# Kernel optimization log

Hardware: AMD Instinct MI355X
Metric: run time of the kernel (lower is better)

The kernel has to match this reference:

```python
import jax, jax.numpy as jnp
import numpy as np

N_NODES = 100000


def setup_inputs() -> dict:
    key = jax.random.key(0)
    k1, k2, k3, k4 = jax.random.split(key, 4)
    E = 1600000
    D_IN, D_OUT = 128, 128
    feat = jax.random.normal(k1, (N_NODES, D_IN), dtype=jnp.float32)
    src = jax.random.randint(k2, (E,), 0, N_NODES, dtype=jnp.int32)
    dst = jax.random.randint(k3, (E,), 0, N_NODES, dtype=jnp.int32)
    # xavier_uniform for weight [in, out]
    limit = float(np.sqrt(6.0 / (D_IN + D_OUT)))
    weight = jax.random.uniform(k4, (D_IN, D_OUT), dtype=jnp.float32,
                                minval=-limit, maxval=limit)
    bias = jnp.zeros((D_OUT,), dtype=jnp.float32)
    return {"feat": feat, "weight": weight, "bias": bias, "src": src, "dst": dst}


def reference(feat, weight, bias, src, dst):
    # in-degree normalization: norm_i = 1/sqrt(in_deg(i)); clamp deg>=1 to avoid inf
    deg = jax.ops.segment_sum(jnp.ones(src.shape[0], dtype=jnp.float32), dst,
                              num_segments=N_NODES)
    norm = jax.lax.rsqrt(jnp.maximum(deg, 1.0))[:, None]  # [N,1]
    h = feat * norm
    # update_all(copy_src, sum): scatter-sum src features into dst nodes (SpMM)
    agg = jax.ops.segment_sum(h[src], dst, num_segments=N_NODES)  # [N, D_in]
    # in_feats == out_feats -> aggregate first, then dense transform
    rst = agg @ weight          # [N, D_out]
    rst = rst * norm + bias
    return rst
```

## Files before the change

kernel.cpp:

```cpp
#include <hip/hip_runtime.h>


constexpr int N_NODES = 100000;
constexpr int D = 128;
constexpr int NB = 256;
constexpr int GROUP = (N_NODES + NB - 1) / NB;
constexpr int CAP = 14336;
constexpr int CONVB = 1280;

typedef float f32x4 __attribute__((ext_vector_type(4)));
typedef short short8 __attribute__((ext_vector_type(8)));
typedef unsigned uint4v __attribute__((ext_vector_type(4)));

__device__ __forceinline__ ushort f2bf(float x) {
    unsigned u = __float_as_uint(x);
    return (ushort)((u + 0x7fffu + ((u >> 16) & 1u)) >> 16);
}
__device__ __forceinline__ float bf2f(ushort h) {
    return __uint_as_float(((unsigned)h) << 16);
}

__global__ __launch_bounds__(256) void p1_histo_conv(const int* __restrict__ dst, int E,
                                                     int* __restrict__ bhist,
                                                     const float* __restrict__ W,
                                                     ushort* __restrict__ whi,
                                                     ushort* __restrict__ wlo,
                                                     const float* __restrict__ feat,
                                                     uint2* __restrict__ ft2) {
    int t = threadIdx.x, blk = blockIdx.x;
    if (blk >= NB) {
        int base = (blk - NB) * 256 + t;
        int stride = CONVB * 256;
        for (int i = base; i < N_NODES * 32; i += stride) {
            f32x4 v = ((const f32x4*)feat)[i];
            uint2 o;
            o.x = (unsigned)f2bf(v[0]) | ((unsigned)f2bf(v[1]) << 16);
            o.y = (unsigned)f2bf(v[2]) | ((unsigned)f2bf(v[3]) << 16);
            ft2[i] = o;
        }
        return;
    }
    __shared__ int h[NB];
    h[t] = 0;
    if (blk < 64) {
        int p = blk * 256 + t;
        int i  = p & 7;
        int l  = (p >> 3) & 63;
        int kt = (p >> 9) & 3;
        int ct = (p >> 11);
        int k = kt * 32 + (l >> 4) * 8 + i;
        int n = ct * 16 + (l & 15);
        float x = W[k * 128 + n];
        ushort hh = f2bf(x);
        whi[p] = hh;
        wlo[p] = f2bf(x - bf2f(hh));
    }
    __syncthreads();
    int per = (E + NB - 1) / NB;
    int s = blk * per, e = min(E, s + per);
    for (int i = s + t; i < e; i += 256) atomicAdd(&h[dst[i] / GROUP], 1);
    __syncthreads();
    bhist[t * NB + blk] = h[t];
}

__global__ __launch_bounds__(256) void p1_scanrow(int* __restrict__ bhist,
                                                  int* __restrict__ rowtot) {
    __shared__ int lds[256];
    int b = blockIdx.x, t = threadIdx.x;
    int v = bhist[b * NB + t];
    lds[t] = v; __syncthreads();
    for (int off = 1; off < 256; off <<= 1) {
        int x = (t >= off) ? lds[t - off] : 0;
        __syncthreads();
        lds[t] += x;
        __syncthreads();
    }
    bhist[b * NB + t] = lds[t] - v;
    if (t == 255) rowtot[b] = lds[255];
}

__global__ __launch_bounds__(256) void p1_scatter(const int* __restrict__ src,
                                                  const int* __restrict__ dst, int E,
                                                  const int* __restrict__ bhist,
                                                  const int* __restrict__ rowtot,
                                                  int* __restrict__ pairs) {
    __shared__ int loff[NB];
    __shared__ int bb[NB];
    int t = threadIdx.x, blk = blockIdx.x;
    int rv = rowtot[t];
    bb[t] = rv; __syncthreads();
    for (int off = 1; off < 256; off <<= 1) {
        int x = (t >= off) ? bb[t - off] : 0;
        __syncthreads();
        bb[t] += x;
        __syncthreads();
    }
    loff[t] = bhist[t * NB + blk] + bb[t] - rv;
    __syncthreads();
    int per = (E + NB - 1) / NB;
    int s = blk * per, e = min(E, s + per);
    for (int i = s + t; i < e; i += 256) {
        int d = dst[i];
        int b = d / GROUP;
        int pos = atomicAdd(&loff[b], 1);
        pairs[pos] = ((d - b * GROUP) << 17) | src[i];
    }
}

__global__ __launch_bounds__(256) void p2_all(const int* __restrict__ pairs,
                                              const int* __restrict__ rowtot,
                                              int* __restrict__ deg,
                                              int* __restrict__ offs,
                                              float* __restrict__ norm,
                                              int* __restrict__ esrc) {
    __shared__ int h[512];
    __shared__ int ssum[256];
    __shared__ int bb[256];
    __shared__ int sbuf[CAP];
    int t = threadIdx.x, b = blockIdx.x;
    int lo = b * GROUP;
    int cnt = min(GROUP, N_NODES - lo);

    int rv = rowtot[t];
    bb[t] = rv;
    h[t] = 0; h[t + 256] = 0;
    __syncthreads();
    for (int off = 1; off < 256; off <<= 1) {
        int x = (t >= off) ? bb[t - off] : 0;
        __syncthreads();
        bb[t] += x;
        __syncthreads();
    }
    int s1 = bb[b];
    int s0 = s1 - rowtot[b];
    __syncthreads();

    for (int i = s0 + t; i < s1; i += 256) atomicAdd(&h[pairs[i] >> 17], 1);
    __syncthreads();

    int v0 = h[2 * t], v1 = h[2 * t + 1];
    int s = v0 + v1;
    ssum[t] = s; __syncthreads();
    for (int off = 1; off < 256; off <<= 1) {
        int x = (t >= off) ? ssum[t - off] : 0;
        __syncthreads();
        ssum[t] += x;
        __syncthreads();
    }
    int pre = ssum[t] - s;
    if (2 * t < cnt) {
        int node = lo + 2 * t;
        deg[node] = v0;
        offs[node] = s0 + pre;
        norm[node] = rsqrtf(fmaxf((float)v0, 1.0f));
    }
    if (2 * t + 1 < cnt) {
        int node = lo + 2 * t + 1;
        deg[node] = v1;
        offs[node] = s0 + pre + v0;
        norm[node] = rsqrtf(fmaxf((float)v1, 1.0f));
    }
    __syncthreads();
    h[2 * t] = pre;
    h[2 * t + 1] = pre + v0;
    __syncthreads();

    int wsize = s1 - s0;
    bool fits = (wsize <= CAP);
    for (int i = s0 + t; i < s1; i += 256) {
        int p = pairs[i];
        int dl = p >> 17;
        int sv = p & 0x1FFFF;
        int pos = atomicAdd(&h[dl], 1);
        if (fits) sbuf[pos] = sv; else esrc[s0 + pos] = sv;
    }
    __syncthreads();
    if (fits)
        for (int i = t; i < wsize; i += 256) esrc[s0 + i] = sbuf[i];
}

__global__ __launch_bounds__(256) void k_gather16(const unsigned* __restrict__ ft,
                                                  const int* __restrict__ offs,
                                                  const int* __restrict__ deg,
                                                  const int* __restrict__ esrc,
                                                  const float* __restrict__ norm,
                                                  unsigned* __restrict__ outbf) {
    int gtid = blockIdx.x * blockDim.x + threadIdx.x;
    int node = gtid >> 6;
    if (node >= N_NODES) return;
    int lane = gtid & 63;
    int g  = lane >> 4;
    int sl = lane & 15;
    int start = offs[node];
    int cnt   = deg[node];
    int last  = start + cnt - 1;
    float acc[8] = {0.f, 0.f, 0.f, 0.f, 0.f, 0.f, 0.f, 0.f};
    const uint4v* ftv = (const uint4v*)ft;
    for (int j = 0; j < cnt; j += 16) {
        int i0 = start + j + g;
        int s0v = esrc[min(i0,      last)];
        int s1v = esrc[min(i0 + 4,  last)];
        int s2v = esrc[min(i0 + 8,  last)];
        int s3v = esrc[min(i0 + 12, last)];
        float w0 = (j + g      < cnt) ? norm[s0v] : 0.0f;
        float w1 = (j + g + 4  < cnt) ? norm[s1v] : 0.0f;
        float w2 = (j + g + 8  < cnt) ? norm[s2v] : 0.0f;
        float w3 = (j + g + 12 < cnt) ? norm[s3v] : 0.0f;
        uint4v u0 = ftv[(size_t)s0v * 16 + sl];
        uint4v u1 = ftv[(size_t)s1v * 16 + sl];
        uint4v u2 = ftv[(size_t)s2v * 16 + sl];
        uint4v u3 = ftv[(size_t)s3v * 16 + sl];
        #pragma unroll
        for (int q = 0; q < 4; ++q) {
            unsigned a = u0[q];
            acc[q * 2]     = fmaf(__uint_as_float(a << 16),         w0, acc[q * 2]);
            acc[q * 2 + 1] = fmaf(__uint_as_float(a & 0xffff0000u), w0, acc[q * 2 + 1]);
        }
        #pragma unroll
        for (int q = 0; q < 4; ++q) {
            unsigned a = u1[q];
            acc[q * 2]     = fmaf(__uint_as_float(a << 16),         w1, acc[q * 2]);
            acc[q * 2 + 1] = fmaf(__uint_as_float(a & 0xffff0000u), w1, acc[q * 2 + 1]);
        }
        #pragma unroll
        for (int q = 0; q < 4; ++q) {
            unsigned a = u2[q];
            acc[q * 2]     = fmaf(__uint_as_float(a << 16),         w2, acc[q * 2]);
            acc[q * 2 + 1] = fmaf(__uint_as_float(a & 0xffff0000u), w2, acc[q * 2 + 1]);
        }
        #pragma unroll
        for (int q = 0; q < 4; ++q) {
            unsigned a = u3[q];
            acc[q * 2]     = fmaf(__uint_as_float(a << 16),         w3, acc[q * 2]);
            acc[q * 2 + 1] = fmaf(__uint_as_float(a & 0xffff0000u), w3, acc[q * 2 + 1]);
        }
    }
    #pragma unroll
    for (int q = 0; q < 8; ++q) {
        acc[q] += __shfl_xor(acc[q], 16, 64);
        acc[q] += __shfl_xor(acc[q], 32, 64);
    }
    if (g == 0) {
        uint4v o;
        #pragma unroll
        for (int q = 0; q < 4; ++q)
            o[q] = (unsigned)f2bf(acc[q * 2]) | ((unsigned)f2bf(acc[q * 2 + 1]) << 16);
        ((uint4v*)outbf)[(size_t)node * 16 + sl] = o;
    }
}

__global__ __launch_bounds__(256) void k_gemm_bf(const ushort* __restrict__ aggbf,
                                                 const ushort* __restrict__ whi,
                                                 const ushort* __restrict__ wlo,
                                                 const float* __restrict__ bias,
                                                 const float* __restrict__ norm,
                                                 float* __restrict__ out) {
    __shared__ ushort sH[16384];
    __shared__ ushort sL[16384];
    {
        const short8* gh = (const short8*)whi;
        const short8* gl = (const short8*)wlo;
        short8* lh = (short8*)sH;
        short8* ll = (short8*)sL;
        for (int i = threadIdx.x; i < 2048; i += 256) { lh[i] = gh[i]; ll[i] = gl[i]; }
    }
    __syncthreads();

    const int lane = threadIdx.x & 63;
    const int wid  = threadIdx.x >> 6;
    const int rsub = lane & 15;
    const int kgrp = lane >> 4;

    const short8* BH = (const short8*)sH;
    const short8* BL = (const short8*)sL;

    const int nstrips = N_NODES / 16;
    for (int strip = blockIdx.x * 4 + wid; strip < nstrips; strip += gridDim.x * 4) {
        const int row0 = strip * 16;
        const ushort* arow = aggbf + (size_t)(row0 + rsub) * D + kgrp * 8;
        short8 a[4];
        #pragma unroll
        for (int kt = 0; kt < 4; ++kt) a[kt] = *(const short8*)(arow + kt * 32);
        float nr[4];
        #pragma unroll
        for (int r = 0; r < 4; ++r) nr[r] = norm[row0 + kgrp * 4 + r];

        #pragma unroll
        for (int ct = 0; ct < 8; ++ct) {
            f32x4 acc = {0.f, 0.f, 0.f, 0.f};
            #pragma unroll
            for (int kt = 0; kt < 4; ++kt) {
                acc = __builtin_amdgcn_mfma_f32_16x16x32_bf16(a[kt], BH[(ct * 4 + kt) * 64 + lane], acc, 0, 0, 0);
                acc = __builtin_amdgcn_mfma_f32_16x16x32_bf16(a[kt], BL[(ct * 4 + kt) * 64 + lane], acc, 0, 0, 0);
            }
            const float bc = bias[ct * 16 + rsub];
            float* ocol = out + (size_t)row0 * D + ct * 16 + rsub;
            #pragma unroll
            for (int r = 0; r < 4; ++r) {
                int row = kgrp * 4 + r;
                ocol[(size_t)row * D] = acc[r] * nr[r] + bc;
            }
        }
    }
}

__global__ void k_scatter(const float* __restrict__ feat, const int* __restrict__ src,
                          const int* __restrict__ dst, const float* __restrict__ norm,
                          int E, float* __restrict__ agg) {
    long long gtid = (long long)blockIdx.x * blockDim.x + threadIdx.x;
    int e    = (int)(gtid >> 6);
    int lane = (int)(gtid & 63);
    if (e >= E) return;
    int s = src[e];
    int t = dst[e];
    float ns = norm[s];
    float2 v = ((const float2*)(feat + (size_t)s * D))[lane];
    float* arow = agg + (size_t)t * D + lane * 2;
    atomicAdd(arow + 0, v.x * ns);
    atomicAdd(arow + 1, v.y * ns);
}
__global__ void k_deg_f(const int* __restrict__ dst, int E, float* __restrict__ deg) {
    int i = blockIdx.x * blockDim.x + threadIdx.x;
    if (i < E) atomicAdd(deg + dst[i], 1.0f);
}
__global__ void k_norm_f(float* __restrict__ dn) {
    int i = blockIdx.x * blockDim.x + threadIdx.x;
    if (i < N_NODES) dn[i] = rsqrtf(fmaxf(dn[i], 1.0f));
}
__global__ __launch_bounds__(256) void k_gemm(float* __restrict__ io,
                                              const float* __restrict__ W,
                                              const float* __restrict__ bias,
                                              const float* __restrict__ norm) {
    __shared__ float sW[D * D];
    __shared__ float srow[2][D];
    for (int i = threadIdx.x; i < D * D; i += 256) sW[i] = W[i];
    const int r = threadIdx.x >> 7;
    const int c = threadIdx.x & 127;
    const float bc = bias[c];
    const int npairs = N_NODES / 2;
    for (int rp = blockIdx.x; rp < npairs; rp += gridDim.x) {
        __syncthreads();
        const int row = rp * 2 + r;
        srow[r][c] = io[(size_t)row * D + c];
        __syncthreads();
        float acc = 0.f;
        #pragma unroll 8
        for (int k = 0; k < D; ++k)
            acc = fmaf(srow[r][k], sW[k * D + c], acc);
        io[(size_t)row * D + c] = acc * norm[row] + bc;
    }
}

extern "C" void kernel_launch(void* const* d_in, const int* in_sizes, int n_in,
                              void* d_out, int out_size, void* d_ws, size_t ws_size,
                              hipStream_t stream) {
    const float* feat   = (const float*)d_in[0];
    const float* weight = (const float*)d_in[1];
    const float* bias   = (const float*)d_in[2];
    const int*   src    = (const int*)d_in[3];
    const int*   dst    = (const int*)d_in[4];
    const int E = in_sizes[3];

    int* pairs = (int*)d_out;

    uintptr_t cur = (uintptr_t)d_ws;
    auto take = [&](size_t bytes) -> void* {
        uintptr_t r = (cur + 63) & ~(uintptr_t)63;
        cur = r + bytes;
        return (void*)r;
    };

    size_t S_ft  = (size_t)N_NODES * 64 * 4;
    size_t S_agg = (size_t)N_NODES * D * 2;
    size_t need  = S_ft + S_agg +
                   (size_t)(3 * N_NODES + 256 + NB * NB + E) * 4 + 65536 + 1024;

    unsigned* ft     = (unsigned*)take(S_ft);
    ushort*   aggbf  = (ushort*)take(S_agg);
    float*    norm   = (float*)take((size_t)N_NODES * 4);
    int*      deg    = (int*)take((size_t)N_NODES * 4);
    int*      offs   = (int*)take((size_t)N_NODES * 4);
    int*      rowtot = (int*)take(256 * 4);
    int*      bhist  = (int*)take((size_t)NB * NB * 4);
    int*      esrc   = (int*)take((size_t)E * 4);
    ushort*   whi    = (ushort*)take(16384 * 2);
    ushort*   wlo    = (ushort*)take(16384 * 2);

    if (ws_size >= need) {
        p1_histo_conv<<<NB + CONVB, 256, 0, stream>>>(dst, E, bhist, weight, whi, wlo,
                                                      feat, (uint2*)ft);
        p1_scanrow<<<NB, 256, 0, stream>>>(bhist, rowtot);
        p1_scatter<<<NB, 256, 0, stream>>>(src, dst, E, bhist, rowtot, pairs);
        p2_all<<<NB, 256, 0, stream>>>(pairs, rowtot, deg, offs, norm, esrc);
        long long gthreads = (long long)N_NODES * 64;
        k_gather16<<<(int)((gthreads + 255) / 256), 256, 0, stream>>>(ft, offs, deg, esrc,
                                                                      norm, (unsigned*)aggbf);
        k_gemm_bf<<<1024, 256, 0, stream>>>(aggbf, whi, wlo, bias, norm, (float*)d_out);
    } else {
        float* agg = (float*)d_out;
        hipMemsetAsync(d_out, 0, (size_t)N_NODES * D * sizeof(float), stream);
        hipMemsetAsync(norm, 0, (size_t)N_NODES * sizeof(float), stream);
        k_deg_f<<<(E + 255) / 256, 256, 0, stream>>>(dst, E, (float*)norm);
        k_norm_f<<<(N_NODES + 255) / 256, 256, 0, stream>>>((float*)norm);
        long long sthreads = (long long)E * 64;
        k_scatter<<<(int)((sthreads + 255) / 256), 256, 0, stream>>>(feat, src, dst, (float*)norm, E, agg);
        k_gemm<<<4096, 256, 0, stream>>>(agg, weight, bias, (float*)norm);
    }
}
```

Measured before the change: 139.0 us.

## Pack fp16 source norm into edge indices and fold row scan into histogram

The scanrow kernel is removed. Row totals are now accumulated with atomics in the histogram kernel, and each scatter block computes its column prefix by serially summing the bhist entries of all earlier blocks. A new pass packs each edge's source norm as fp16 into the upper 15 bits of its esrc entry, so the gather no longer does a dependent random load of norm[src]. In exchange it adds a memset, an extra pass over all edges, an O(NB) loop per scatter thread, and reduced precision on the norm weights, since the top bit of the half is dropped and only positive values are assumed.

```diff
diff --git a/kernel.cpp b/kernel.cpp
--- a/kernel.cpp
+++ b/kernel.cpp
@@ -1,4 +1,5 @@
 #include <hip/hip_runtime.h>
+#include <hip/hip_fp16.h>
 
 
 constexpr int N_NODES = 100000;
@@ -19,9 +20,15 @@
 __device__ __forceinline__ float bf2f(ushort h) {
     return __uint_as_float(((unsigned)h) << 16);
 }
+__device__ __forceinline__ float dec_h15(int p) {
+    unsigned short b = (unsigned short)((unsigned)p >> 17);
+    __half hh; __builtin_memcpy(&hh, &b, 2);
+    return __half2float(hh);
+}
 
 __global__ __launch_bounds__(256) void p1_histo_conv(const int* __restrict__ dst, int E,
                                                      int* __restrict__ bhist,
+                                                     int* __restrict__ rowtot,
                                                      const float* __restrict__ W,
                                                      ushort* __restrict__ whi,
                                                      ushort* __restrict__ wlo,
@@ -60,23 +67,8 @@
     int s = blk * per, e = min(E, s + per);
     for (int i = s + t; i < e; i += 256) atomicAdd(&h[dst[i] / GROUP], 1);
     __syncthreads();
-    bhist[t * NB + blk] = h[t];
-}
-
-__global__ __launch_bounds__(256) void p1_scanrow(int* __restrict__ bhist,
-                                                  int* __restrict__ rowtot) {
-    __shared__ int lds[256];
-    int b = blockIdx.x, t = threadIdx.x;
-    int v = bhist[b * NB + t];
-    lds[t] = v; __syncthreads();
-    for (int off = 1; off < 256; off <<= 1) {
-        int x = (t >= off) ? lds[t - off] : 0;
-        __syncthreads();
-        lds[t] += x;
-        __syncthreads();
-    }
-    bhist[b * NB + t] = lds[t] - v;
-    if (t == 255) rowtot[b] = lds[255];
+    bhist[blk * NB + t] = h[t];
+    if (h[t]) atomicAdd(&rowtot[t], h[t]);
 }
 
 __global__ __launch_bounds__(256) void p1_scatter(const int* __restrict__ src,
@@ -95,7 +87,9 @@
         bb[t] += x;
         __syncthreads();
     }
-    loff[t] = bhist[t * NB + blk] + bb[t] - rv;
+    int cp = 0;
+    for (int c = 0; c < blk; ++c) cp += bhist[c * NB + t];
+    loff[t] = cp + bb[t] - rv;
     __syncthreads();
     int per = (E + NB - 1) / NB;
     int s = blk * per, e = min(E, s + per);
@@ -179,11 +173,20 @@
         for (int i = t; i < wsize; i += 256) esrc[s0 + i] = sbuf[i];
 }
 
+__global__ void k_enorm(int* __restrict__ esrc, const float* __restrict__ norm, int E) {
+    int i = blockIdx.x * blockDim.x + threadIdx.x;
+    if (i < E) {
+        int s = esrc[i];
+        __half hh = __float2half(norm[s]);
+        unsigned short b; __builtin_memcpy(&b, &hh, 2);
+        esrc[i] = ((int)b << 17) | s;
+    }
+}
+
 __global__ __launch_bounds__(256) void k_gather16(const unsigned* __restrict__ ft,
                                                   const int* __restrict__ offs,
                                                   const int* __restrict__ deg,
                                                   const int* __restrict__ esrc,
-                                                  const float* __restrict__ norm,
                                                   unsigned* __restrict__ outbf) {
     int gtid = blockIdx.x * blockDim.x + threadIdx.x;
     int node = gtid >> 6;
@@ -198,14 +201,18 @@
     const uint4v* ftv = (const uint4v*)ft;
     for (int j = 0; j < cnt; j += 16) {
         int i0 = start + j + g;
-        int s0v = esrc[min(i0,      last)];
-        int s1v = esrc[min(i0 + 4,  last)];
-        int s2v = esrc[min(i0 + 8,  last)];
-        int s3v = esrc[min(i0 + 12, last)];
-        float w0 = (j + g      < cnt) ? norm[s0v] : 0.0f;
-        float w1 = (j + g + 4  < cnt) ? norm[s1v] : 0.0f;
-        float w2 = (j + g + 8  < cnt) ? norm[s2v] : 0.0f;
-        float w3 = (j + g + 12 < cnt) ? norm[s3v] : 0.0f;
+        int p0 = esrc[min(i0,      last)];
+        int p1 = esrc[min(i0 + 4,  last)];
+        int p2 = esrc[min(i0 + 8,  last)];
+        int p3 = esrc[min(i0 + 12, last)];
+        int s0v = p0 & 0x1FFFF;
+        int s1v = p1 & 0x1FFFF;
+        int s2v = p2 & 0x1FFFF;
+        int s3v = p3 & 0x1FFFF;
+        float w0 = (j + g      < cnt) ? dec_h15(p0) : 0.0f;
+        float w1 = (j + g + 4  < cnt) ? dec_h15(p1) : 0.0f;
+        float w2 = (j + g + 8  < cnt) ? dec_h15(p2) : 0.0f;
+        float w3 = (j + g + 12 < cnt) ? dec_h15(p3) : 0.0f;
         uint4v u0 = ftv[(size_t)s0v * 16 + sl];
         uint4v u1 = ftv[(size_t)s1v * 16 + sl];
         uint4v u2 = ftv[(size_t)s2v * 16 + sl];
@@ -387,14 +394,15 @@
     ushort*   wlo    = (ushort*)take(16384 * 2);
 
     if (ws_size >= need) {
-        p1_histo_conv<<<NB + CONVB, 256, 0, stream>>>(dst, E, bhist, weight, whi, wlo,
+        hipMemsetAsync(rowtot, 0, 256 * sizeof(int), stream);
+        p1_histo_conv<<<NB + CONVB, 256, 0, stream>>>(dst, E, bhist, rowtot, weight, whi, wlo,
                                                       feat, (uint2*)ft);
-        p1_scanrow<<<NB, 256, 0, stream>>>(bhist, rowtot);
         p1_scatter<<<NB, 256, 0, stream>>>(src, dst, E, bhist, rowtot, pairs);
         p2_all<<<NB, 256, 0, stream>>>(pairs, rowtot, deg, offs, norm, esrc);
+        k_enorm<<<(E + 255) / 256, 256, 0, stream>>>(esrc, norm, E);
         long long gthreads = (long long)N_NODES * 64;
         k_gather16<<<(int)((gthreads + 255) / 256), 256, 0, stream>>>(ft, offs, deg, esrc,
-                                                                      norm, (unsigned*)aggbf);
+                                                                      (unsigned*)aggbf);
         k_gemm_bf<<<1024, 256, 0, stream>>>(aggbf, whi, wlo, bias, norm, (float*)d_out);
     } else {
         float* agg = (float*)d_out;
```

Result: slower. 178.7 us (+28.5%).

## Fuse neighbor gather and bf16 MFMA GEMM into one kernel via LDS tile

Applied to the files above, without the earlier changes.

Merges the gather-aggregate kernel and the dense GEMM kernel into one. Each block aggregates 16 nodes, four per wave, into a padded LDS bf16 tile. After a barrier, each wave computes two 16-column output tiles with MFMA, reading the weight fragments directly from global memory instead of staging them in LDS. This removes the round trip of the bf16 aggregate buffer through global memory and one kernel launch. The cost is less latency hiding per wave during the gather, the block-wide barrier, and repeated global loads of the weights in every block.

```diff
diff --git a/kernel.cpp b/kernel.cpp
--- a/kernel.cpp
+++ b/kernel.cpp
@@ -7,6 +7,7 @@
 constexpr int GROUP = (N_NODES + NB - 1) / NB;
 constexpr int CAP = 14336;
 constexpr int CONVB = 1280;
+constexpr int RPAD = 136;
 
 typedef float f32x4 __attribute__((ext_vector_type(4)));
 typedef short short8 __attribute__((ext_vector_type(8)));
@@ -179,127 +180,112 @@
         for (int i = t; i < wsize; i += 256) esrc[s0 + i] = sbuf[i];
 }
 
-__global__ __launch_bounds__(256) void k_gather16(const unsigned* __restrict__ ft,
-                                                  const int* __restrict__ offs,
-                                                  const int* __restrict__ deg,
-                                                  const int* __restrict__ esrc,
-                                                  const float* __restrict__ norm,
-                                                  unsigned* __restrict__ outbf) {
-    int gtid = blockIdx.x * blockDim.x + threadIdx.x;
-    int node = gtid >> 6;
-    if (node >= N_NODES) return;
-    int lane = gtid & 63;
-    int g  = lane >> 4;
-    int sl = lane & 15;
-    int start = offs[node];
-    int cnt   = deg[node];
-    int last  = start + cnt - 1;
-    float acc[8] = {0.f, 0.f, 0.f, 0.f, 0.f, 0.f, 0.f, 0.f};
+__global__ __launch_bounds__(256) void k_gather_gemm(const unsigned* __restrict__ ft,
+                                                     const int* __restrict__ offs,
+                                                     const int* __restrict__ deg,
+                                                     const int* __restrict__ esrc,
+                                                     const float* __restrict__ norm,
+                                                     const ushort* __restrict__ whi,
+                                                     const ushort* __restrict__ wlo,
+                                                     const float* __restrict__ bias,
+                                                     float* __restrict__ out) {
+    __shared__ ushort sA[16 * RPAD];
+    const int wid  = threadIdx.x >> 6;
+    const int lane = threadIdx.x & 63;
+    const int g  = lane >> 4;
+    const int sl = lane & 15;
+    const int row0 = blockIdx.x * 16;
     const uint4v* ftv = (const uint4v*)ft;
-    for (int j = 0; j < cnt; j += 16) {
-        int i0 = start + j + g;
-        int s0v = esrc[min(i0,      last)];
-        int s1v = esrc[min(i0 + 4,  last)];
-        int s2v = esrc[min(i0 + 8,  last)];
-        int s3v = esrc[min(i0 + 12, last)];
-        float w0 = (j + g      < cnt) ? norm[s0v] : 0.0f;
-        float w1 = (j + g + 4  < cnt) ? norm[s1v] : 0.0f;
-        float w2 = (j + g + 8  < cnt) ? norm[s2v] : 0.0f;
-        float w3 = (j + g + 12 < cnt) ? norm[s3v] : 0.0f;
-        uint4v u0 = ftv[(size_t)s0v * 16 + sl];
-        uint4v u1 = ftv[(size_t)s1v * 16 + sl];
-        uint4v u2 = ftv[(size_t)s2v * 16 + sl];
-        uint4v u3 = ftv[(size_t)s3v * 16 + sl];
+
+    #pragma unroll
+    for (int n4 = 0; n4 < 4; ++n4) {
+        int n = wid * 4 + n4;
+        int node = row0 + n;
+        int start = offs[node];
+        int cnt   = deg[node];
+        int last  = start + cnt - 1;
+        float acc[8] = {0.f, 0.f, 0.f, 0.f, 0.f, 0.f, 0.f, 0.f};
+        for (int j = 0; j < cnt; j += 16) {
+            int i0 = start + j + g;
+            int s0v = esrc[min(i0,      last)];
+            int s1v = esrc[min(i0 + 4,  last)];
+            int s2v = esrc[min(i0 + 8,  last)];
+            int s3v = esrc[min(i0 + 12, last)];
+            float w0 = (j + g      < cnt) ? norm[s0v] : 0.0f;
+            float w1 = (j + g + 4  < cnt) ? norm[s1v] : 0.0f;
+            float w2 = (j + g + 8  < cnt) ? norm[s2v] : 0.0f;
+            float w3 = (j + g + 12 < cnt) ? norm[s3v] : 0.0f;
+            uint4v u0 = ftv[(size_t)s0v * 16 + sl];
+            uint4v u1 = ftv[(size_t)s1v * 16 + sl];
+            uint4v u2 = ftv[(size_t)s2v * 16 + sl];
+            uint4v u3 = ftv[(size_t)s3v * 16 + sl];
+            #pragma unroll
+            for (int q = 0; q < 4; ++q) {
+                unsigned a = u0[q];
+                acc[q * 2]     = fmaf(__uint_as_float(a << 16),         w0, acc[q * 2]);
+                acc[q * 2 + 1] = fmaf(__uint_as_float(a & 0xffff0000u), w0, acc[q * 2 + 1]);
+            }
+            #pragma unroll
+            for (int q = 0; q < 4; ++q) {
+                unsigned a = u1[q];
+                acc[q * 2]     = fmaf(__uint_as_float(a << 16),         w1, acc[q * 2]);
+                acc[q * 2 + 1] = fmaf(__uint_as_float(a & 0xffff0000u), w1, acc[q * 2 + 1]);
+            }
+            #pragma unroll
+            for (int q = 0; q < 4; ++q) {
+                unsigned a = u2[q];
+                acc[q * 2]     = fmaf(__uint_as_float(a << 16),         w2, acc[q * 2]);
+                acc[q * 2 + 1] = fmaf(__uint_as_float(a & 0xffff0000u), w2, acc[q * 2 + 1]);
+            }
+            #pragma unroll
+            for (int q = 0; q < 4; ++q) {
+                unsigned a = u3[q];
+                acc[q * 2]     = fmaf(__uint_as_float(a << 16),         w3, acc[q * 2]);
+                acc[q * 2 + 1] = fmaf(__uint_as_float(a & 0xffff0000u), w3, acc[q * 2 + 1]);
+            }
+        }
         #pragma unroll
-        for (int q = 0; q < 4; ++q) {
-            unsigned a = u0[q];
-            acc[q * 2]     = fmaf(__uint_as_float(a << 16),         w0, acc[q * 2]);
-            acc[q * 2 + 1] = fmaf(__uint_as_float(a & 0xffff0000u), w0, acc[q * 2 + 1]);
-        }
-        #pragma unroll
-        for (int q = 0; q < 4; ++q) {
-            unsigned a = u1[q];
-            acc[q * 2]     = fmaf(__uint_as_float(a << 16),         w1, acc[q * 2]);
-            acc[q * 2 + 1] = fmaf(__uint_as_float(a & 0xffff0000u), w1, acc[q * 2 + 1]);
-        }
-        #pragma unroll
-        for (int q = 0; q < 4; ++q) {
-            unsigned a = u2[q];
-            acc[q * 2]     = fmaf(__uint_as_float(a << 16),         w2, acc[q * 2]);
-            acc[q * 2 + 1] = fmaf(__uint_as_float(a & 0xffff0000u), w2, acc[q * 2 + 1]);
-        }
-        #pragma unroll
-        for (int q = 0; q < 4; ++q) {
-            unsigned a = u3[q];
-            acc[q * 2]     = fmaf(__uint_as_float(a << 16),         w3, acc[q * 2]);
-            acc[q * 2 + 1] = fmaf(__uint_as_float(a & 0xffff0000u), w3, acc[q * 2 + 1]);
-        }
-    }
-    #pragma unroll
-    for (int q = 0; q < 8; ++q) {
-        acc[q] += __shfl_xor(acc[q], 16, 64);
-        acc[q] += __shfl_xor(acc[q], 32, 64);
-    }
-    if (g == 0) {
-        uint4v o;
-        #pragma unroll
-        for (int q = 0; q < 4; ++q)
-            o[q] = (unsigned)f2bf(acc[q * 2]) | ((unsigned)f2bf(acc[q * 2 + 1]) << 16);
-        ((uint4v*)outbf)[(size_t)node * 16 + sl] = o;
-    }
-}
-
-__global__ __launch_bounds__(256) void k_gemm_bf(const ushort* __restrict__ aggbf,
-                                                 const ushort* __restrict__ whi,
-                                                 const ushort* __restrict__ wlo,
-                                                 const float* __restrict__ bias,
-                                                 const float* __restrict__ norm,
-                                                 float* __restrict__ out) {
-    __shared__ ushort sH[16384];
-    __shared__ ushort sL[16384];
-    {
-        const short8* gh = (const short8*)whi;
-        const short8* gl = (const short8*)wlo;
-        short8* lh = (short8*)sH;
-        short8* ll = (short8*)sL;
-        for (int i = threadIdx.x; i < 2048; i += 256) { lh[i] = gh[i]; ll[i] = gl[i]; }
-    }
-    __syncthreads();
-
-    const int lane = threadIdx.x & 63;
-    const int wid  = threadIdx.x >> 6;
+        for (int q = 0; q < 8; ++q) {
+            acc[q] += __shfl_xor(acc[q], 16, 64);
+            acc[q] += __shfl_xor(acc[q], 32, 64);
+        }
+        if (g == 0) {
+            uint4v o;
+            #pragma unroll
+            for (int q = 0; q < 4; ++q)
+                o[q] = (unsigned)f2bf(acc[q * 2]) | ((unsigned)f2bf(acc[q * 2 + 1]) << 16);
+            *(uint4v*)(&sA[n * RPAD + sl * 8]) = o;
+        }
+    }
+    __syncthreads();
+
     const int rsub = lane & 15;
     const int kgrp = lane >> 4;
-
-    const short8* BH = (const short8*)sH;
-    const short8* BL = (const short8*)sL;
-
-    const int nstrips = N_NODES / 16;
-    for (int strip = blockIdx.x * 4 + wid; strip < nstrips; strip += gridDim.x * 4) {
-        const int row0 = strip * 16;
-        const ushort* arow = aggbf + (size_t)(row0 + rsub) * D + kgrp * 8;
-        short8 a[4];
+    short8 a[4];
+    #pragma unroll
+    for (int kt = 0; kt < 4; ++kt)
+        a[kt] = *(const short8*)(&sA[rsub * RPAD + kt * 32 + kgrp * 8]);
+    float nr[4];
+    #pragma unroll
+    for (int r = 0; r < 4; ++r) nr[r] = norm[row0 + kgrp * 4 + r];
+
+    const short8* BH = (const short8*)whi;
+    const short8* BL = (const short8*)wlo;
+    #pragma unroll
+    for (int cc = 0; cc < 2; ++cc) {
+        int ct = wid * 2 + cc;
+        f32x4 acc = {0.f, 0.f, 0.f, 0.f};
         #pragma unroll
-        for (int kt = 0; kt < 4; ++kt) a[kt] = *(const short8*)(arow + kt * 32);
-        float nr[4];
+        for (int kt = 0; kt < 4; ++kt) {
+            acc = __builtin_amdgcn_mfma_f32_16x16x32_bf16(a[kt], BH[(ct * 4 + kt) * 64 + lane], acc, 0, 0, 0);
+            acc = __builtin_amdgcn_mfma_f32_16x16x32_bf16(a[kt], BL[(ct * 4 + kt) * 64 + lane], acc, 0, 0, 0);
+        }
+        const float bc = bias[ct * 16 + rsub];
+        float* ocol = out + (size_t)row0 * D + ct * 16 + rsub;
         #pragma unroll
-        for (int r = 0; r < 4; ++r) nr[r] = norm[row0 + kgrp * 4 + r];
-
-        #pragma unroll
-        for (int ct = 0; ct < 8; ++ct) {
-            f32x4 acc = {0.f, 0.f, 0.f, 0.f};
-            #pragma unroll
-            for (int kt = 0; kt < 4; ++kt) {
-                acc = __builtin_amdgcn_mfma_f32_16x16x32_bf16(a[kt], BH[(ct * 4 + kt) * 64 + lane], acc, 0, 0, 0);
-                acc = __builtin_amdgcn_mfma_f32_16x16x32_bf16(a[kt], BL[(ct * 4 + kt) * 64 + lane], acc, 0, 0, 0);
-            }
-            const float bc = bias[ct * 16 + rsub];
-            float* ocol = out + (size_t)row0 * D + ct * 16 + rsub;
-            #pragma unroll
-            for (int r = 0; r < 4; ++r) {
-                int row = kgrp * 4 + r;
-                ocol[(size_t)row * D] = acc[r] * nr[r] + bc;
-            }
+        for (int r = 0; r < 4; ++r) {
+            int row = kgrp * 4 + r;
+            ocol[(size_t)row * D] = acc[r] * nr[r] + bc;
         }
     }
 }
@@ -371,12 +357,10 @@
     };
 
     size_t S_ft  = (size_t)N_NODES * 64 * 4;
-    size_t S_agg = (size_t)N_NODES * D * 2;
-    size_t need  = S_ft + S_agg +
+    size_t need  = S_ft +
                    (size_t)(3 * N_NODES + 256 + NB * NB + E) * 4 + 65536 + 1024;
 
     unsigned* ft     = (unsigned*)take(S_ft);
-    ushort*   aggbf  = (ushort*)take(S_agg);
     float*    norm   = (float*)take((size_t)N_NODES * 4);
     int*      deg    = (int*)take((size_t)N_NODES * 4);
     int*      offs   = (int*)take((size_t)N_NODES * 4);
@@ -392,10 +376,8 @@
         p1_scanrow<<<NB, 256, 0, stream>>>(bhist, rowtot);
         p1_scatter<<<NB, 256, 0, stream>>>(src, dst, E, bhist, rowtot, pairs);
         p2_all<<<NB, 256, 0, stream>>>(pairs, rowtot, deg, offs, norm, esrc);
-        long long gthreads = (long long)N_NODES * 64;
-        k_gather16<<<(int)((gthreads + 255) / 256), 256, 0, stream>>>(ft, offs, deg, esrc,
-                                                                      norm, (unsigned*)aggbf);
-        k_gemm_bf<<<1024, 256, 0, stream>>>(aggbf, whi, wlo, bias, norm, (float*)d_out);
+        k_gather_gemm<<<N_NODES / 16, 256, 0, stream>>>(ft, offs, deg, esrc, norm,
+                                                        whi, wlo, bias, (float*)d_out);
     } else {
         float* agg = (float*)d_out;
         hipMemsetAsync(d_out, 0, (size_t)N_NODES * D * sizeof(float), stream);
```

New measurement: 133.7 us, median of 2. -3.8%, faster.
